# Optimization experiments

Measured on AMD Instinct MI355X. Metric: run time of the kernel, lower is better.

Reference implementation:

```python
import jax, jax.numpy as jnp
import numpy as np

B, F, T, N, A, E_INC, NUM_EDGES, C_OUT = 32, 64, 20, 512, 64, 2048, 128, 128
C_IN = F + A


def setup_inputs() -> dict:
    key = jax.random.key(0)
    k = jax.random.split(key, 6)
    x = jax.random.normal(k[0], (B, F, T, N), dtype=jnp.float32)
    H = jax.random.randint(k[1], (B, T, 2, E_INC), 0, NUM_EDGES)  # row0: node ids, row1: hyperedge ids
    ssa = jax.random.normal(k[2], (B, T, N, A), dtype=jnp.float32)
    W = jax.random.uniform(k[3], (B, T, E_INC), dtype=jnp.float32)  # unused by conv (matches original)
    theta = jax.random.normal(k[4], (C_OUT, C_IN), dtype=jnp.float32) / np.sqrt(C_IN).astype(np.float32)
    bias = jnp.zeros((C_OUT,), dtype=jnp.float32)
    return {"x": x, "H": H, "ssa": ssa, "W": W, "theta": theta, "bias": bias}


def _hconv(feat, hidx, theta, bias):
    # One PyG HypergraphConv (no attention, unit hyperedge weights):
    #   out = D^{-1} H B^{-1} H^T (X Theta^T) + b
    # feat: [N, C_in], hidx: [2, E_inc]
    node_idx, edge_idx = hidx[0], hidx[1]
    xp = feat @ theta.T  # [N, C_out]
    ones = jnp.ones(node_idx.shape, dtype=xp.dtype)
    deg_n = jax.ops.segment_sum(ones, node_idx, num_segments=N)         # D
    deg_e = jax.ops.segment_sum(ones, edge_idx, num_segments=NUM_EDGES)  # B
    Dinv = jnp.where(deg_n > 0, 1.0 / deg_n, 0.0)
    Binv = jnp.where(deg_e > 0, 1.0 / deg_e, 0.0)
    # node -> hyperedge aggregation
    edge_feat = Binv[:, None] * jax.ops.segment_sum(xp[node_idx], edge_idx, num_segments=NUM_EDGES)
    # hyperedge -> node aggregation
    out = Dinv[:, None] * jax.ops.segment_sum(edge_feat[edge_idx], node_idx, num_segments=N)
    return out + bias


def reference(x, H, ssa, W, theta, bias):
    # x: [B, F, T, N] -> [B, T, N, F], concat scene attention -> [B, T, N, C_in]
    feat = jnp.concatenate([jnp.transpose(x, (0, 2, 3, 1)), ssa], axis=-1)
    conv = lambda f, h: _hconv(f, h, theta, bias)
    out = jax.vmap(jax.vmap(conv))(feat, H)  # [B, T, N, C_out]
    # Original does a raw .reshape(B, C_out, T, N) (NOT a permute) -- replicate exactly.
    return out.reshape(B, C_OUT, T, N)
```

## Files before the change

kernel.cpp:

```cpp
#include <hip/hip_runtime.h>
#include <cstdint>
#include <cstddef>

namespace {

constexpr int B_ = 32, F_ = 64, T_ = 20, N_ = 512, A_ = 64;
constexpr int EINC = 2048, NEDGE = 128, COUT = 128, CIN = 128;
constexpr int THREADS = 1024;
constexpr int NBT = B_ * T_;

constexpr int L_SRT8 = 0;
constexpr int L_OFN  = 512;
constexpr int L_XQ   = 1028;
constexpr int L_DGE  = 1028;
constexpr int L_CUE  = 1156;
constexpr int L_OFE  = 1284;
constexpr int L_DGN  = 1416;
constexpr int L_CUN  = 1928;
constexpr int L_ESR  = 2440;
constexpr int L_EQ   = 3464;
constexpr int L_ST   = 5512;
constexpr int L_HST  = 17924;
constexpr int L_CRS  = 17988;
constexpr int L_PRM  = 18052;
constexpr int XQS    = 132;
constexpr int LDS_WORDS = 18180;
constexpr int LDS_BYTES = LDS_WORDS * 4;

typedef unsigned u32x8 __attribute__((ext_vector_type(8)));
typedef float f32x4v __attribute__((ext_vector_type(4)));
typedef short bf16x8v __attribute__((ext_vector_type(8)));

__device__ inline unsigned short f2bf(float f) {
    unsigned int u = __float_as_uint(f);
    u = u + 0x7FFFu + ((u >> 16) & 1u);
    return (unsigned short)(u >> 16);
}
__device__ inline unsigned packbf(float lo, float hi) {
    return ((unsigned)f2bf(hi) << 16) | (unsigned)f2bf(lo);
}
__device__ inline float bflo(unsigned p) { return __uint_as_float(p << 16); }
__device__ inline float bfhi(unsigned p) { return __uint_as_float(p & 0xFFFF0000u); }

#define LOAD_CHUNK(CC, DST) do {                                              \
    const int c_ = (CC);                                                      \
    if (c_ < 4) {                                                             \
        const float* xr_ = x + (((size_t)b * F_ + c_ * 16) * T_ + t) * N_ + n; \
        _Pragma("unroll")                                                     \
        for (int m_ = 0; m_ < 8; ++m_) {                                      \
            float f0_ = xr_[(size_t)(2 * m_) * (T_ * N_)];                    \
            float f1_ = xr_[(size_t)(2 * m_ + 1) * (T_ * N_)];                \
            DST[m_] = packbf(f0_, f1_);                                       \
        }                                                                     \
    } else {                                                                  \
        const float* sr_ = ssa + ((size_t)bt * N_ + n) * A_ + (c_ - 4) * 16;  \
        _Pragma("unroll")                                                     \
        for (int m_ = 0; m_ < 4; ++m_) {                                      \
            float4 u_ = *(const float4*)(sr_ + 4 * m_);                       \
            DST[2 * m_]     = packbf(u_.x, u_.y);                             \
            DST[2 * m_ + 1] = packbf(u_.z, u_.w);                             \
        }                                                                     \
    }                                                                         \
} while (0)

__global__ __launch_bounds__(256)
void theta_pack(const float* __restrict__ theta, unsigned* __restrict__ ws) {
    int w = blockIdx.x * 256 + threadIdx.x;
    int f = w >> 8, rem = w & 255;
    int l = rem >> 2, kq = rem & 3;
    int kk = f & 3, ct = f >> 2;
    int co = ct * 16 + (l & 15);
    int ci = kk * 32 + (l >> 4) * 8 + kq * 2;
    const float2 tv = *(const float2*)(theta + (size_t)co * CIN + ci);
    ws[w] = packbf(tv.x, tv.y);
}

template<bool HAS_WS>
__global__ __launch_bounds__(THREADS, 8)
void hgconv(const float* __restrict__ x, const int* __restrict__ H,
            const float* __restrict__ ssa, const float* __restrict__ theta,
            const float* __restrict__ bias, float* __restrict__ out,
            const unsigned* __restrict__ thw)
{
    extern __shared__ float sf[];
    int* si = (int*)sf;

    const int tid = (int)threadIdx.x;
    const int bt  = (int)blockIdx.x;
    const int b   = bt / T_;
    const int t   = bt - b * T_;

    unsigned char*  s_srt8  = (unsigned char*)(si + L_SRT8);
    int*            s_ofn   = si + L_OFN;
    int*            s_ofe   = si + L_OFE;
    int*            s_dge   = si + L_DGE;
    int*            s_cue   = si + L_CUE;
    int*            s_dgn   = si + L_DGN;
    int*            s_cun   = si + L_CUN;
    unsigned short* s_esr16 = (unsigned short*)(si + L_ESR);
    unsigned*       s_eq16  = (unsigned*)(si + L_EQ);
    unsigned*       s_st16  = (unsigned*)(si + L_ST);
    int*            s_nid   = si + L_EQ;
    int*            s_eid   = si + L_ST;
    int*            s_hst   = si + L_HST;
    int*            s_crs   = si + L_CRS;
    int*            s_prm   = si + L_PRM;
    float*          s_xq    = sf + L_XQ;

    const int n  = tid & (N_ - 1);
    const int hf = tid >> 9;

    const int* Hb = H + (size_t)bt * (2 * EINC);
    #pragma unroll
    for (int k = 0; k < EINC / THREADS; ++k) {
        int i = tid + k * THREADS;
        s_nid[i] = Hb[i];
        s_eid[i] = Hb[EINC + i];
    }
    if (tid < N_)    s_dgn[tid] = 0;
    if (tid < NEDGE) s_dge[tid] = 0;
    if (tid < 64)    s_hst[tid] = 0;
    __syncthreads();

    #pragma unroll
    for (int k = 0; k < EINC / THREADS; ++k) {
        int i = tid + k * THREADS;
        atomicAdd(&s_dgn[s_nid[i]], 1);
        atomicAdd(&s_dge[s_eid[i]], 1);
    }
    __syncthreads();

    const bool act = s_dgn[n] > 0;
    u32x8 vv;
    if (act) LOAD_CHUNK(hf, vv);

    if (tid < 64) {
        const int ll = tid;
        int d0 = s_dge[2 * ll], d1 = s_dge[2 * ll + 1];
        int run = d0 + d1;
        int scan = run;
        #pragma unroll
        for (int d = 1; d < 64; d <<= 1) {
            int o = __shfl_up(scan, d);
            if (ll >= d) scan += o;
        }
        int excl = scan - run;
        s_ofe[2 * ll] = excl;
        s_ofe[2 * ll + 1] = excl + d0;
        if (ll == 63) s_ofe[NEDGE] = scan;
    } else if (tid < 128) {
        const int ll = tid & 63;
        int v, loc[8], run = 0;
        #pragma unroll
        for (int qq = 0; qq < 8; ++qq) { v = s_dgn[ll * 8 + qq]; loc[qq] = run; run += v; }
        int scan = run;
        #pragma unroll
        for (int d = 1; d < 64; d <<= 1) {
            int o = __shfl_up(scan, d);
            if (ll >= d) scan += o;
        }
        int excl = scan - run;
        #pragma unroll
        for (int qq = 0; qq < 8; ++qq) s_ofn[ll * 8 + qq] = excl + loc[qq];
        if (ll == 63) s_ofn[N_] = scan;
    }
    __syncthreads();

    if (tid < N_)    s_cun[tid] = s_ofn[tid];
    if (tid < NEDGE) {
        s_cue[tid] = s_ofe[tid];
        int d = s_dge[tid];
        atomicAdd(&s_hst[63 - (d < 63 ? d : 63)], 1);
    }
    __syncthreads();

    #pragma unroll
    for (int k = 0; k < EINC / THREADS; ++k) {
        int i = tid + k * THREADS;
        int nd = s_nid[i];
        int e  = s_eid[i];
        int pe = atomicAdd(&s_cue[e], 1);
        s_esr16[pe] = (unsigned short)nd;
        int pn = atomicAdd(&s_cun[nd], 1);
        s_srt8[pn] = (unsigned char)e;
    }
    if (tid < 64) {
        int h = s_hst[tid];
        int scan = h;
        #pragma unroll
        for (int d = 1; d < 64; d <<= 1) {
            int o = __shfl_up(scan, d);
            if (tid >= d) scan += o;
        }
        s_crs[tid] = scan - h;
    }
    __syncthreads();

    const int eg = tid >> 3;
    const int ep = tid & 7;
    const int wv = tid >> 6, l = tid & 63;
    const int q  = l >> 4, lco = l & 15;
    const int rt = wv >> 1;
    const int cth = (wv & 1) * 4;
    const int ar = rt * 16 + lco;
    const int aoff = ar * 16 + ((4 * q) ^ ((ar & 3) << 2));

    f32x4v acc[4];
    #pragma unroll
    for (int i = 0; i < 4; ++i) acc[i] = (f32x4v){0.f, 0.f, 0.f, 0.f};

    #pragma unroll
    for (int r = 0; r < 4; ++r) {
        if (act) {
            #pragma unroll
            for (int p2 = 0; p2 < 4; ++p2) {
                int P = 4 * hf + p2;
                unsigned* sp = s_st16 + n * 16 + ((2 * P) ^ ((n & 7) << 1));
                *(uint2*)sp = make_uint2(vv[2 * p2], vv[2 * p2 + 1]);
            }
        }
        if (r == 0 && tid < NEDGE) {
            int d = s_dge[tid];
            int pos = atomicAdd(&s_crs[63 - (d < 63 ? d : 63)], 1);
            s_prm[pos] = tid;
        }
        __syncthreads();

        if (r < 3 && act) LOAD_CHUNK(2 * r + 2 + hf, vv);

        {
            int pe  = s_prm[eg];
            int gk0 = s_ofe[pe];
            int gd  = s_dge[pe];
            int gk1 = gk0 + gd;
            float gbinv = (gd > 0) ? 1.0f / (float)gd : 0.0f;
            float a0 = 0.f, a1 = 0.f, a2 = 0.f, a3 = 0.f;
            for (int k = gk0; k < gk1; ++k) {
                int nd = (int)s_esr16[k];
                uint2 pr = *(const uint2*)(s_st16 + nd * 16
                                + ((2 * ep) ^ ((nd & 7) << 1)));
                a0 += bflo(pr.x); a1 += bfhi(pr.x);
                a2 += bflo(pr.y); a3 += bfhi(pr.y);
            }
            unsigned* qp = s_eq16 + pe * 16 + ((2 * ep) ^ ((pe & 3) << 2));
            *(uint2*)qp = make_uint2(packbf(a0 * gbinv, a1 * gbinv),
                                     packbf(a2 * gbinv, a3 * gbinv));
        }
        __syncthreads();

        {
            bf16x8v av = *(const bf16x8v*)(s_eq16 + aoff);
            if (HAS_WS) {
                #pragma unroll
                for (int i = 0; i < 4; ++i) {
                    uint4 u = ((const uint4*)thw)[((cth + i) * 4 + r) * 64 + l];
                    acc[i] = __builtin_amdgcn_mfma_f32_16x16x32_bf16(
                        av, *(const bf16x8v*)&u, acc[i], 0, 0, 0);
                }
            } else {
                #pragma unroll
                for (int i = 0; i < 4; ++i) {
                    const float* tp = theta + (size_t)((cth + i) * 16 + lco) * CIN
                                    + r * 32 + q * 8;
                    float4 t0 = *(const float4*)tp;
                    float4 t1 = *(const float4*)(tp + 4);
                    unsigned pw[4] = { packbf(t0.x, t0.y), packbf(t0.z, t0.w),
                                       packbf(t1.x, t1.y), packbf(t1.z, t1.w) };
                    acc[i] = __builtin_amdgcn_mfma_f32_16x16x32_bf16(
                        av, *(const bf16x8v*)pw, acc[i], 0, 0, 0);
                }
            }
        }
    }
    __syncthreads();

    #pragma unroll
    for (int i = 0; i < 4; ++i) {
        const int co = (cth + i) * 16 + lco;
        #pragma unroll
        for (int reg = 0; reg < 4; ++reg)
            s_xq[(rt * 16 + q * 4 + reg) * XQS + co] = acc[i][reg];
    }
    __syncthreads();

    {
        const int lw = tid & 31;
        const int g  = tid >> 5;
        float4 bsv = *(const float4*)(bias + 4 * lw);
        for (int nn = g; nn < N_; nn += 32) {
            int o0 = s_ofn[nn], o1 = s_ofn[nn + 1];
            float f0 = 0.f, f1 = 0.f, f2 = 0.f, f3 = 0.f;
            for (int k = o0; k < o1; ++k) {
                int e = (int)s_srt8[k];
                float4 v = *(const float4*)(s_xq + e * XQS + 4 * lw);
                f0 += v.x; f1 += v.y; f2 += v.z; f3 += v.w;
            }
            float dinv = (o1 > o0) ? 1.0f / (float)(o1 - o0) : 0.0f;
            float* op = out + ((size_t)bt * N_ + nn) * COUT + 4 * lw;
            *(float4*)op = make_float4(f0 * dinv + bsv.x, f1 * dinv + bsv.y,
                                       f2 * dinv + bsv.z, f3 * dinv + bsv.w);
        }
    }
}

}

extern "C" void kernel_launch(void* const* d_in, const int* in_sizes, int n_in,
                              void* d_out, int out_size, void* d_ws, size_t ws_size,
                              hipStream_t stream) {
    const float* x     = (const float*)d_in[0];
    const int*   H     = (const int*)d_in[1];
    const float* ssa   = (const float*)d_in[2];
    const float* theta = (const float*)d_in[4];
    const float* bias  = (const float*)d_in[5];
    float* outp = (float*)d_out;

    const bool use_ws = (d_ws != nullptr) && (ws_size >= 32768);
    if (use_ws) {
        hipLaunchKernelGGL(theta_pack, dim3(32), dim3(256), 0, stream,
                           theta, (unsigned*)d_ws);
        (void)hipFuncSetAttribute((const void*)&hgconv<true>,
                                  hipFuncAttributeMaxDynamicSharedMemorySize, LDS_BYTES);
        hipLaunchKernelGGL(hgconv<true>, dim3(NBT), dim3(THREADS), LDS_BYTES,
                           stream, x, H, ssa, theta, bias, outp,
                           (const unsigned*)d_ws);
    } else {
        (void)hipFuncSetAttribute((const void*)&hgconv<false>,
                                  hipFuncAttributeMaxDynamicSharedMemorySize, LDS_BYTES);
        hipLaunchKernelGGL(hgconv<false>, dim3(NBT), dim3(THREADS), LDS_BYTES,
                           stream, x, H, ssa, theta, bias, outp, nullptr);
    }
}
```

Before: 74.73 us.

## Make the hypergraph conv kernel persistent with an atomic work queue

Launches a fixed grid of 512 blocks instead of one block per (b,t) slice. After finishing a slice, each block pulls the next slice index from a global atomic counter that the theta packing kernel seeds in the workspace. This aims to cut the cost of scheduling a second partial wave of blocks and to balance uneven per-slice work dynamically. It also drops the per-node activity guard on feature loads, so every node's chunk is loaded unconditionally. The costs are an extra global atomic and two block barriers per slice, and a larger required workspace.

Measured after the change: 167.1 us. +123.6%, slower.

```diff
diff --git a/kernel.cpp b/kernel.cpp
--- a/kernel.cpp
+++ b/kernel.cpp
@@ -8,9 +8,11 @@
 constexpr int EINC = 2048, NEDGE = 128, COUT = 128, CIN = 128;
 constexpr int THREADS = 1024;
 constexpr int NBT = B_ * T_;
+constexpr int GRID_WS = 512;
 
 constexpr int L_SRT8 = 0;
 constexpr int L_OFN  = 512;
+constexpr int L_NXT  = 1026;
 constexpr int L_XQ   = 1028;
 constexpr int L_DGE  = 1028;
 constexpr int L_CUE  = 1156;
@@ -73,6 +75,7 @@
     int ci = kk * 32 + (l >> 4) * 8 + kq * 2;
     const float2 tv = *(const float2*)(theta + (size_t)co * CIN + ci);
     ws[w] = packbf(tv.x, tv.y);
+    if (w == 0) ws[8192] = (unsigned)GRID_WS;
 }
 
 template<bool HAS_WS>
@@ -80,15 +83,12 @@
 void hgconv(const float* __restrict__ x, const int* __restrict__ H,
             const float* __restrict__ ssa, const float* __restrict__ theta,
             const float* __restrict__ bias, float* __restrict__ out,
-            const unsigned* __restrict__ thw)
+            const unsigned* __restrict__ thw, unsigned* __restrict__ wq)
 {
     extern __shared__ float sf[];
     int* si = (int*)sf;
 
     const int tid = (int)threadIdx.x;
-    const int bt  = (int)blockIdx.x;
-    const int b   = bt / T_;
-    const int t   = bt - b * T_;
 
     unsigned char*  s_srt8  = (unsigned char*)(si + L_SRT8);
     int*            s_ofn   = si + L_OFN;
@@ -110,92 +110,6 @@
     const int n  = tid & (N_ - 1);
     const int hf = tid >> 9;
 
-    const int* Hb = H + (size_t)bt * (2 * EINC);
-    #pragma unroll
-    for (int k = 0; k < EINC / THREADS; ++k) {
-        int i = tid + k * THREADS;
-        s_nid[i] = Hb[i];
-        s_eid[i] = Hb[EINC + i];
-    }
-    if (tid < N_)    s_dgn[tid] = 0;
-    if (tid < NEDGE) s_dge[tid] = 0;
-    if (tid < 64)    s_hst[tid] = 0;
-    __syncthreads();
-
-    #pragma unroll
-    for (int k = 0; k < EINC / THREADS; ++k) {
-        int i = tid + k * THREADS;
-        atomicAdd(&s_dgn[s_nid[i]], 1);
-        atomicAdd(&s_dge[s_eid[i]], 1);
-    }
-    __syncthreads();
-
-    const bool act = s_dgn[n] > 0;
-    u32x8 vv;
-    if (act) LOAD_CHUNK(hf, vv);
-
-    if (tid < 64) {
-        const int ll = tid;
-        int d0 = s_dge[2 * ll], d1 = s_dge[2 * ll + 1];
-        int run = d0 + d1;
-        int scan = run;
-        #pragma unroll
-        for (int d = 1; d < 64; d <<= 1) {
-            int o = __shfl_up(scan, d);
-            if (ll >= d) scan += o;
-        }
-        int excl = scan - run;
-        s_ofe[2 * ll] = excl;
-        s_ofe[2 * ll + 1] = excl + d0;
-        if (ll == 63) s_ofe[NEDGE] = scan;
-    } else if (tid < 128) {
-        const int ll = tid & 63;
-        int v, loc[8], run = 0;
-        #pragma unroll
-        for (int qq = 0; qq < 8; ++qq) { v = s_dgn[ll * 8 + qq]; loc[qq] = run; run += v; }
-        int scan = run;
-        #pragma unroll
-        for (int d = 1; d < 64; d <<= 1) {
-            int o = __shfl_up(scan, d);
-            if (ll >= d) scan += o;
-        }
-        int excl = scan - run;
-        #pragma unroll
-        for (int qq = 0; qq < 8; ++qq) s_ofn[ll * 8 + qq] = excl + loc[qq];
-        if (ll == 63) s_ofn[N_] = scan;
-    }
-    __syncthreads();
-
-    if (tid < N_)    s_cun[tid] = s_ofn[tid];
-    if (tid < NEDGE) {
-        s_cue[tid] = s_ofe[tid];
-        int d = s_dge[tid];
-        atomicAdd(&s_hst[63 - (d < 63 ? d : 63)], 1);
-    }
-    __syncthreads();
-
-    #pragma unroll
-    for (int k = 0; k < EINC / THREADS; ++k) {
-        int i = tid + k * THREADS;
-        int nd = s_nid[i];
-        int e  = s_eid[i];
-        int pe = atomicAdd(&s_cue[e], 1);
-        s_esr16[pe] = (unsigned short)nd;
-        int pn = atomicAdd(&s_cun[nd], 1);
-        s_srt8[pn] = (unsigned char)e;
-    }
-    if (tid < 64) {
-        int h = s_hst[tid];
-        int scan = h;
-        #pragma unroll
-        for (int d = 1; d < 64; d <<= 1) {
-            int o = __shfl_up(scan, d);
-            if (tid >= d) scan += o;
-        }
-        s_crs[tid] = scan - h;
-    }
-    __syncthreads();
-
     const int eg = tid >> 3;
     const int ep = tid & 7;
     const int wv = tid >> 6, l = tid & 63;
@@ -205,101 +119,205 @@
     const int ar = rt * 16 + lco;
     const int aoff = ar * 16 + ((4 * q) ^ ((ar & 3) << 2));
 
-    f32x4v acc[4];
-    #pragma unroll
-    for (int i = 0; i < 4; ++i) acc[i] = (f32x4v){0.f, 0.f, 0.f, 0.f};
-
-    #pragma unroll
-    for (int r = 0; r < 4; ++r) {
-        if (act) {
-            #pragma unroll
-            for (int p2 = 0; p2 < 4; ++p2) {
-                int P = 4 * hf + p2;
-                unsigned* sp = s_st16 + n * 16 + ((2 * P) ^ ((n & 7) << 1));
-                *(uint2*)sp = make_uint2(vv[2 * p2], vv[2 * p2 + 1]);
-            }
-        }
-        if (r == 0 && tid < NEDGE) {
+    int bt = (int)blockIdx.x;
+
+    for (;;) {
+        const int b = bt / T_;
+        const int t = bt - b * T_;
+
+        const int* Hb = H + (size_t)bt * (2 * EINC);
+        #pragma unroll
+        for (int k = 0; k < EINC / THREADS; ++k) {
+            int i = tid + k * THREADS;
+            s_nid[i] = Hb[i];
+            s_eid[i] = Hb[EINC + i];
+        }
+        if (tid < N_)    s_dgn[tid] = 0;
+        if (tid < NEDGE) s_dge[tid] = 0;
+        if (tid < 64)    s_hst[tid] = 0;
+        __syncthreads();
+
+        #pragma unroll
+        for (int k = 0; k < EINC / THREADS; ++k) {
+            int i = tid + k * THREADS;
+            atomicAdd(&s_dgn[s_nid[i]], 1);
+            atomicAdd(&s_dge[s_eid[i]], 1);
+        }
+        __syncthreads();
+
+        u32x8 vv;
+        LOAD_CHUNK(hf, vv);
+
+        if (tid < 64) {
+            const int ll = tid;
+            int d0 = s_dge[2 * ll], d1 = s_dge[2 * ll + 1];
+            int run = d0 + d1;
+            int scan = run;
+            #pragma unroll
+            for (int d = 1; d < 64; d <<= 1) {
+                int o = __shfl_up(scan, d);
+                if (ll >= d) scan += o;
+            }
+            int excl = scan - run;
+            s_ofe[2 * ll] = excl;
+            s_ofe[2 * ll + 1] = excl + d0;
+            if (ll == 63) s_ofe[NEDGE] = scan;
+        } else if (tid < 128) {
+            const int ll = tid & 63;
+            int v, loc[8], run = 0;
+            #pragma unroll
+            for (int qq = 0; qq < 8; ++qq) { v = s_dgn[ll * 8 + qq]; loc[qq] = run; run += v; }
+            int scan = run;
+            #pragma unroll
+            for (int d = 1; d < 64; d <<= 1) {
+                int o = __shfl_up(scan, d);
+                if (ll >= d) scan += o;
+            }
+            int excl = scan - run;
+            #pragma unroll
+            for (int qq = 0; qq < 8; ++qq) s_ofn[ll * 8 + qq] = excl + loc[qq];
+            if (ll == 63) s_ofn[N_] = scan;
+        }
+        __syncthreads();
+
+        if (tid < N_)    s_cun[tid] = s_ofn[tid];
+        if (tid < NEDGE) {
+            s_cue[tid] = s_ofe[tid];
             int d = s_dge[tid];
-            int pos = atomicAdd(&s_crs[63 - (d < 63 ? d : 63)], 1);
-            s_prm[pos] = tid;
-        }
-        __syncthreads();
-
-        if (r < 3 && act) LOAD_CHUNK(2 * r + 2 + hf, vv);
+            atomicAdd(&s_hst[63 - (d < 63 ? d : 63)], 1);
+        }
+        __syncthreads();
+
+        #pragma unroll
+        for (int k = 0; k < EINC / THREADS; ++k) {
+            int i = tid + k * THREADS;
+            int nd = s_nid[i];
+            int e  = s_eid[i];
+            int pe = atomicAdd(&s_cue[e], 1);
+            s_esr16[pe] = (unsigned short)nd;
+            int pn = atomicAdd(&s_cun[nd], 1);
+            s_srt8[pn] = (unsigned char)e;
+        }
+        if (tid < 64) {
+            int h = s_hst[tid];
+            int scan = h;
+            #pragma unroll
+            for (int d = 1; d < 64; d <<= 1) {
+                int o = __shfl_up(scan, d);
+                if (tid >= d) scan += o;
+            }
+            s_crs[tid] = scan - h;
+        }
+        __syncthreads();
+
+        f32x4v ac0 = {0.f,0.f,0.f,0.f}, ac1 = {0.f,0.f,0.f,0.f};
+        f32x4v ac2 = {0.f,0.f,0.f,0.f}, ac3 = {0.f,0.f,0.f,0.f};
+
+        #pragma unroll
+        for (int r = 0; r < 4; ++r) {
+            {
+                #pragma unroll
+                for (int p2 = 0; p2 < 4; ++p2) {
+                    int P = 4 * hf + p2;
+                    unsigned* sp = s_st16 + n * 16 + ((2 * P) ^ ((n & 7) << 1));
+                    *(uint2*)sp = make_uint2(vv[2 * p2], vv[2 * p2 + 1]);
+                }
+            }
+            if (r == 0 && tid < NEDGE) {
+                int d = s_dge[tid];
+                int pos = atomicAdd(&s_crs[63 - (d < 63 ? d : 63)], 1);
+                s_prm[pos] = tid;
+            }
+            __syncthreads();
+
+            if (r < 3) LOAD_CHUNK(2 * r + 2 + hf, vv);
+
+            {
+                int pe  = s_prm[eg];
+                int gk0 = s_ofe[pe];
+                int gd  = s_dge[pe];
+                int gk1 = gk0 + gd;
+                float gbinv = (gd > 0) ? 1.0f / (float)gd : 0.0f;
+                float a0 = 0.f, a1 = 0.f, a2 = 0.f, a3 = 0.f;
+                for (int k = gk0; k < gk1; ++k) {
+                    int nd = (int)s_esr16[k];
+                    uint2 pr = *(const uint2*)(s_st16 + nd * 16
+                                    + ((2 * ep) ^ ((nd & 7) << 1)));
+                    a0 += bflo(pr.x); a1 += bfhi(pr.x);
+                    a2 += bflo(pr.y); a3 += bfhi(pr.y);
+                }
+                unsigned* qp = s_eq16 + pe * 16 + ((2 * ep) ^ ((pe & 3) << 2));
+                *(uint2*)qp = make_uint2(packbf(a0 * gbinv, a1 * gbinv),
+                                         packbf(a2 * gbinv, a3 * gbinv));
+            }
+            __syncthreads();
+
+            {
+                bf16x8v av = *(const bf16x8v*)(s_eq16 + aoff);
+                if (HAS_WS) {
+                    const uint4* t4 = (const uint4*)thw;
+                    uint4 u0 = t4[((cth + 0) * 4 + r) * 64 + l];
+                    uint4 u1 = t4[((cth + 1) * 4 + r) * 64 + l];
+                    uint4 u2 = t4[((cth + 2) * 4 + r) * 64 + l];
+                    uint4 u3 = t4[((cth + 3) * 4 + r) * 64 + l];
+                    ac0 = __builtin_amdgcn_mfma_f32_16x16x32_bf16(av, *(const bf16x8v*)&u0, ac0, 0, 0, 0);
+                    ac1 = __builtin_amdgcn_mfma_f32_16x16x32_bf16(av, *(const bf16x8v*)&u1, ac1, 0, 0, 0);
+                    ac2 = __builtin_amdgcn_mfma_f32_16x16x32_bf16(av, *(const bf16x8v*)&u2, ac2, 0, 0, 0);
+                    ac3 = __builtin_amdgcn_mfma_f32_16x16x32_bf16(av, *(const bf16x8v*)&u3, ac3, 0, 0, 0);
+                } else {
+                    #pragma unroll
+                    for (int i = 0; i < 4; ++i) {
+                        const float* tp = theta + (size_t)((cth + i) * 16 + lco) * CIN
+                                        + r * 32 + q * 8;
+                        float4 t0 = *(const float4*)tp;
+                        float4 t1 = *(const float4*)(tp + 4);
+                        unsigned pw[4] = { packbf(t0.x, t0.y), packbf(t0.z, t0.w),
+                                           packbf(t1.x, t1.y), packbf(t1.z, t1.w) };
+                        f32x4v& ac = (i == 0) ? ac0 : (i == 1) ? ac1 : (i == 2) ? ac2 : ac3;
+                        ac = __builtin_amdgcn_mfma_f32_16x16x32_bf16(
+                            av, *(const bf16x8v*)pw, ac, 0, 0, 0);
+                    }
+                }
+            }
+        }
+        __syncthreads();
+
+        #pragma unroll
+        for (int reg = 0; reg < 4; ++reg) {
+            const int row = (rt * 16 + q * 4 + reg) * XQS;
+            s_xq[row + (cth + 0) * 16 + lco] = ac0[reg];
+            s_xq[row + (cth + 1) * 16 + lco] = ac1[reg];
+            s_xq[row + (cth + 2) * 16 + lco] = ac2[reg];
+            s_xq[row + (cth + 3) * 16 + lco] = ac3[reg];
+        }
+        __syncthreads();
 
         {
-            int pe  = s_prm[eg];
-            int gk0 = s_ofe[pe];
-            int gd  = s_dge[pe];
-            int gk1 = gk0 + gd;
-            float gbinv = (gd > 0) ? 1.0f / (float)gd : 0.0f;
-            float a0 = 0.f, a1 = 0.f, a2 = 0.f, a3 = 0.f;
-            for (int k = gk0; k < gk1; ++k) {
-                int nd = (int)s_esr16[k];
-                uint2 pr = *(const uint2*)(s_st16 + nd * 16
-                                + ((2 * ep) ^ ((nd & 7) << 1)));
-                a0 += bflo(pr.x); a1 += bfhi(pr.x);
-                a2 += bflo(pr.y); a3 += bfhi(pr.y);
-            }
-            unsigned* qp = s_eq16 + pe * 16 + ((2 * ep) ^ ((pe & 3) << 2));
-            *(uint2*)qp = make_uint2(packbf(a0 * gbinv, a1 * gbinv),
-                                     packbf(a2 * gbinv, a3 * gbinv));
-        }
-        __syncthreads();
-
-        {
-            bf16x8v av = *(const bf16x8v*)(s_eq16 + aoff);
-            if (HAS_WS) {
-                #pragma unroll
-                for (int i = 0; i < 4; ++i) {
-                    uint4 u = ((const uint4*)thw)[((cth + i) * 4 + r) * 64 + l];
-                    acc[i] = __builtin_amdgcn_mfma_f32_16x16x32_bf16(
-                        av, *(const bf16x8v*)&u, acc[i], 0, 0, 0);
+            const int lw = tid & 31;
+            const int g  = tid >> 5;
+            float4 bsv = *(const float4*)(bias + 4 * lw);
+            for (int nn = g; nn < N_; nn += 32) {
+                int o0 = s_ofn[nn], o1 = s_ofn[nn + 1];
+                float f0 = 0.f, f1 = 0.f, f2 = 0.f, f3 = 0.f;
+                for (int k = o0; k < o1; ++k) {
+                    int e = (int)s_srt8[k];
+                    float4 v = *(const float4*)(s_xq + e * XQS + 4 * lw);
+                    f0 += v.x; f1 += v.y; f2 += v.z; f3 += v.w;
                 }
-            } else {
-                #pragma unroll
-                for (int i = 0; i < 4; ++i) {
-                    const float* tp = theta + (size_t)((cth + i) * 16 + lco) * CIN
-                                    + r * 32 + q * 8;
-                    float4 t0 = *(const float4*)tp;
-                    float4 t1 = *(const float4*)(tp + 4);
-                    unsigned pw[4] = { packbf(t0.x, t0.y), packbf(t0.z, t0.w),
-                                       packbf(t1.x, t1.y), packbf(t1.z, t1.w) };
-                    acc[i] = __builtin_amdgcn_mfma_f32_16x16x32_bf16(
-                        av, *(const bf16x8v*)pw, acc[i], 0, 0, 0);
-                }
-            }
-        }
-    }
-    __syncthreads();
-
-    #pragma unroll
-    for (int i = 0; i < 4; ++i) {
-        const int co = (cth + i) * 16 + lco;
-        #pragma unroll
-        for (int reg = 0; reg < 4; ++reg)
-            s_xq[(rt * 16 + q * 4 + reg) * XQS + co] = acc[i][reg];
-    }
-    __syncthreads();
-
-    {
-        const int lw = tid & 31;
-        const int g  = tid >> 5;
-        float4 bsv = *(const float4*)(bias + 4 * lw);
-        for (int nn = g; nn < N_; nn += 32) {
-            int o0 = s_ofn[nn], o1 = s_ofn[nn + 1];
-            float f0 = 0.f, f1 = 0.f, f2 = 0.f, f3 = 0.f;
-            for (int k = o0; k < o1; ++k) {
-                int e = (int)s_srt8[k];
-                float4 v = *(const float4*)(s_xq + e * XQS + 4 * lw);
-                f0 += v.x; f1 += v.y; f2 += v.z; f3 += v.w;
-            }
-            float dinv = (o1 > o0) ? 1.0f / (float)(o1 - o0) : 0.0f;
-            float* op = out + ((size_t)bt * N_ + nn) * COUT + 4 * lw;
-            *(float4*)op = make_float4(f0 * dinv + bsv.x, f1 * dinv + bsv.y,
-                                       f2 * dinv + bsv.z, f3 * dinv + bsv.w);
-        }
+                float dinv = (o1 > o0) ? 1.0f / (float)(o1 - o0) : 0.0f;
+                float* op = out + ((size_t)bt * N_ + nn) * COUT + 4 * lw;
+                *(float4*)op = make_float4(f0 * dinv + bsv.x, f1 * dinv + bsv.y,
+                                           f2 * dinv + bsv.z, f3 * dinv + bsv.w);
+            }
+        }
+
+        if (!HAS_WS) break;
+
+        __syncthreads();
+        if (tid == 0) si[L_NXT] = (int)atomicAdd(wq, 1u);
+        __syncthreads();
+        bt = __builtin_amdgcn_readfirstlane(si[L_NXT]);
+        if (bt >= NBT) break;
     }
 }
 
@@ -315,19 +333,19 @@
     const float* bias  = (const float*)d_in[5];
     float* outp = (float*)d_out;
 
-    const bool use_ws = (d_ws != nullptr) && (ws_size >= 32768);
+    const bool use_ws = (d_ws != nullptr) && (ws_size >= 32772);
     if (use_ws) {
         hipLaunchKernelGGL(theta_pack, dim3(32), dim3(256), 0, stream,
                            theta, (unsigned*)d_ws);
         (void)hipFuncSetAttribute((const void*)&hgconv<true>,
                                   hipFuncAttributeMaxDynamicSharedMemorySize, LDS_BYTES);
-        hipLaunchKernelGGL(hgconv<true>, dim3(NBT), dim3(THREADS), LDS_BYTES,
+        hipLaunchKernelGGL(hgconv<true>, dim3(GRID_WS), dim3(THREADS), LDS_BYTES,
                            stream, x, H, ssa, theta, bias, outp,
-                           (const unsigned*)d_ws);
+                           (const unsigned*)d_ws, (unsigned*)d_ws + 8192);
     } else {
         (void)hipFuncSetAttribute((const void*)&hgconv<false>,
                                   hipFuncAttributeMaxDynamicSharedMemorySize, LDS_BYTES);
         hipLaunchKernelGGL(hgconv<false>, dim3(NBT), dim3(THREADS), LDS_BYTES,
-                           stream, x, H, ssa, theta, bias, outp, nullptr);
+                           stream, x, H, ssa, theta, bias, outp, nullptr, nullptr);
     }
 }
```
